# Optimization experiments

Hardware: AMD Instinct MI355X
Metric: run time of the kernel (lower is better)

Reference implementation:

```python
import jax, jax.numpy as jnp
import numpy as np

N = 4096      # number of nodes (len(batch_node))
K = 8         # number of adjacency channels
C = 256       # in_channels == out_channels
E = 131072    # number of edges (avg degree 32)


def setup_inputs() -> dict:
    key = jax.random.key(0)
    k1, k2, k3 = jax.random.split(key, 3)
    h = jax.random.normal(k1, (C, N), dtype=jnp.float32)
    X = jax.random.normal(k2, (E, K), dtype=jnp.float32)
    # sample unique (src, dst) pairs so the scatter-set has no duplicate writes
    rng = np.random.default_rng(0)
    flat = rng.choice(N * N, size=E, replace=False)
    edge_index = jnp.asarray(np.stack([flat // N, flat % N]).astype(np.int32))
    batch_node = jnp.zeros((N,), dtype=jnp.float32)
    # glorot uniform: stdv = sqrt(6 / (in + out))
    stdv = np.sqrt(6.0 / (C + C)).astype(np.float32)
    weight = jax.random.uniform(k3, (K, C, C), dtype=jnp.float32,
                                minval=-stdv, maxval=stdv)
    bias = jnp.zeros((C,), dtype=jnp.float32)
    return {"h": h, "X": X, "edge_index": edge_index,
            "batch_node": batch_node, "weight": weight, "bias": bias}


def reference(h, X, edge_index, batch_node, weight, bias):
    Kk = weight.shape[0]
    Nn = batch_node.shape[0]
    # scatter edge features into K dense [N, N] adjacency tensors
    resx = jnp.zeros((Kk, Nn, Nn), dtype=h.dtype)
    resx = resx.at[:, edge_index[0], edge_index[1]].set(X.T)
    # res[k] = h @ resx[k] : [K, C, N]
    res = jnp.einsum('cn,knm->kcm', h, resx)
    # sum_k weight[k] @ res[k] : [C, N]  (in_channels == out_channels)
    out = jnp.einsum('kio,kon->in', weight, res)
    # (res.T + bias).T == res + bias[:, None]
    return out + bias[:, None]
```

## Files before the change

### kernel.cpp

```cpp
#include <hip/hip_runtime.h>

constexpr int NN = 4096;
constexpr int KC = 8;
constexpr int CC = 256;
constexpr int NE = 131072;
constexpr int KK = KC * CC;
constexpr int CAP = 96;

typedef short bf16x8 __attribute__((ext_vector_type(8)));
typedef float f32x4 __attribute__((ext_vector_type(4)));

__device__ inline unsigned short f2bf(float f) {
    union { float f; unsigned int u; } v; v.f = f;
    unsigned int u = v.u;
    u += 0x7fffu + ((u >> 16) & 1u);
    return (unsigned short)(u >> 16);
}
__device__ inline float bf2f(unsigned short u) {
    union { unsigned int i; float f; } w; w.i = ((unsigned int)u) << 16; return w.f;
}

__global__ __launch_bounds__(256) void k_prep(
    const float* __restrict__ h, const float* __restrict__ w,
    unsigned short* __restrict__ ht, unsigned short* __restrict__ A,
    int* __restrict__ cursor) {
    int b = blockIdx.x;
    int t = threadIdx.x;
    if (b < 1024) {
        __shared__ float tile[32][33];
        int nb = b >> 3, cb = b & 7;
        int n0 = nb * 32, c0 = cb * 32;
        int tx = t & 31, ty = t >> 5;
#pragma unroll
        for (int j = 0; j < 32; j += 8)
            tile[ty + j][tx] = h[(size_t)(c0 + ty + j) * NN + n0 + tx];
        __syncthreads();
#pragma unroll
        for (int j = 0; j < 32; j += 8)
            ht[(size_t)(n0 + ty + j) * CC + c0 + tx] = f2bf(tile[tx][ty + j]);
    } else {
        int idx = (b - 1024) * 256 + t;
        if (idx < NN) cursor[idx] = 0;
        int o = idx & 255;
        int k = (idx >> 8) & 7;
        int i = idx >> 11;
        A[idx] = f2bf(w[(k << 16) | (i << 8) | o]);
    }
}

__global__ void k_fill(const int* __restrict__ edge_src, const int* __restrict__ edge_dst,
                       int* __restrict__ cursor, int2* __restrict__ bins) {
    int e = blockIdx.x * 256 + threadIdx.x;
    int d = edge_dst[e];
    int slot = atomicAdd(&cursor[d], 1);
    if (slot < CAP) bins[d * CAP + slot] = make_int2(e, edge_src[e]);
}

__device__ inline void agg_accum(f32x4 acc[KC], float4 v, float4 xa, float4 xb) {
    f32x4 vv = {v.x, v.y, v.z, v.w};
    acc[0] += xa.x * vv; acc[1] += xa.y * vv;
    acc[2] += xa.z * vv; acc[3] += xa.w * vv;
    acc[4] += xb.x * vv; acc[5] += xb.y * vv;
    acc[6] += xb.z * vv; acc[7] += xb.w * vv;
}

__global__ __launch_bounds__(256) void k_agg(
    const int* __restrict__ cursor, const int2* __restrict__ bins,
    const float* __restrict__ X, const unsigned short* __restrict__ ht,
    unsigned short* __restrict__ agg) {
    const int wid  = __builtin_amdgcn_readfirstlane(threadIdx.x >> 6);
    const int lane = threadIdx.x & 63;
    const int n = blockIdx.x * 4 + wid;
    int cnt = cursor[n];
    cnt = cnt > CAP ? CAP : cnt;
    const int p0 = n * CAP;
    const int p1 = p0 + cnt;
    const float4* X4 = reinterpret_cast<const float4*>(X);

    f32x4 acc[KC] = {};

    int p = p0;
    for (; p + 8 <= p1; p += 8) {
        int2 q[8];
        ushort4 u[8];
#pragma unroll
        for (int j = 0; j < 8; ++j) q[j] = bins[p + j];
#pragma unroll
        for (int j = 0; j < 8; ++j)
            u[j] = *(const ushort4*)(ht + (size_t)q[j].y * CC + 4 * lane);
#pragma unroll
        for (int j = 0; j < 8; ++j) {
            float4 v = {bf2f(u[j].x), bf2f(u[j].y), bf2f(u[j].z), bf2f(u[j].w)};
            agg_accum(acc, v, X4[q[j].x * 2], X4[q[j].x * 2 + 1]);
        }
    }
    for (; p < p1; ++p) {
        int2 q = bins[p];
        ushort4 u = *(const ushort4*)(ht + (size_t)q.y * CC + 4 * lane);
        float4 v = {bf2f(u.x), bf2f(u.y), bf2f(u.z), bf2f(u.w)};
        agg_accum(acc, v, X4[q.x * 2], X4[q.x * 2 + 1]);
    }

    unsigned short* op = agg + (size_t)n * KK + 4 * lane;
#pragma unroll
    for (int k = 0; k < KC; ++k) {
        ushort4 w;
        w.x = f2bf(acc[k][0]); w.y = f2bf(acc[k][1]);
        w.z = f2bf(acc[k][2]); w.w = f2bf(acc[k][3]);
        *reinterpret_cast<ushort4*>(op + k * CC) = w;
    }
}

__global__ __launch_bounds__(256) void k_gemm_mfma(
    const unsigned short* __restrict__ A, const unsigned short* __restrict__ B,
    const float* __restrict__ bias, float* __restrict__ out) {
    constexpr int BM = 64, BN = 32, BK = 64;
    constexpr int NT = KK / BK;
    __shared__ unsigned short As[2][BM][BK];
    __shared__ unsigned short Bs[2][BN][BK];
    const int tid  = threadIdx.x;
    const int wid  = tid >> 6;
    const int lane = tid & 63;

    const int raw = blockIdx.x;
    const int swz = (raw & 7) * 64 + (raw >> 3);
    const int i0 = (swz & 3) * BM;
    const int n0 = (swz >> 2) * BN;

    const int wm = (wid & 1) * 32;
    const int wn = (wid >> 1) * 16;

    const int lrow = lane >> 3;
    const int csrc = ((lane & 7) ^ lrow) * 8;

    f32x4 acc[2] = {};

#define STAGE(T, BUF)                                                              \
    do {                                                                           \
        int kc0_ = (T) * BK;                                                       \
        _Pragma("unroll")                                                          \
        for (int q = 0; q < 2; ++q) {                                              \
            int seg = wid + q * 4;                                                 \
            int row = seg * 8 + lrow;                                              \
            __builtin_amdgcn_global_load_lds(                                      \
                (const __attribute__((address_space(1))) void*)(                   \
                    A + (size_t)(i0 + row) * KK + kc0_ + csrc),                    \
                (__attribute__((address_space(3))) void*)(                         \
                    (char*)&As[BUF][0][0] + seg * 1024), 16, 0, 0);                \
        }                                                                          \
        {                                                                          \
            int row = wid * 8 + lrow;                                              \
            __builtin_amdgcn_global_load_lds(                                      \
                (const __attribute__((address_space(1))) void*)(                   \
                    B + (size_t)(n0 + row) * KK + kc0_ + csrc),                    \
                (__attribute__((address_space(3))) void*)(                         \
                    (char*)&Bs[BUF][0][0] + wid * 1024), 16, 0, 0);                \
        }                                                                          \
    } while (0)

    STAGE(0, 0);

    const int rA = wm + (lane & 15);
    const int rB = wn + (lane & 15);
    const int sw = lane & 7;
    const int chb = lane >> 4;

    for (int t = 0; t < NT; ++t) {
        int b = t & 1;
        if (t + 1 < NT) {
            STAGE(t + 1, b ^ 1);
            asm volatile("s_waitcnt vmcnt(3)" ::: "memory");
        } else {
            asm volatile("s_waitcnt vmcnt(0)" ::: "memory");
        }
        __builtin_amdgcn_s_barrier();
        asm volatile("" ::: "memory");

        const char* Ab = (const char*)&As[b][0][0];
        const char* Bb = (const char*)&Bs[b][0][0];
#pragma unroll
        for (int ks = 0; ks < BK; ks += 32) {
            const int ch = (ks >> 3) + chb;
            bf16x8 a0 = *(const bf16x8*)(Ab + rA * 128 + ((ch ^ sw) << 4));
            bf16x8 a1 = *(const bf16x8*)(Ab + (rA + 16) * 128 + ((ch ^ sw) << 4));
            bf16x8 b0 = *(const bf16x8*)(Bb + rB * 128 + ((ch ^ sw) << 4));
            acc[0] = __builtin_amdgcn_mfma_f32_16x16x32_bf16(a0, b0, acc[0], 0, 0, 0);
            acc[1] = __builtin_amdgcn_mfma_f32_16x16x32_bf16(a1, b0, acc[1], 0, 0, 0);
        }
        asm volatile("" ::: "memory");
        __builtin_amdgcn_s_barrier();
    }
#undef STAGE

    const int lr = (lane >> 4) * 4;
    const int lc = lane & 15;
#pragma unroll
    for (int mi = 0; mi < 2; ++mi) {
#pragma unroll
        for (int r = 0; r < 4; ++r) {
            int i = i0 + wm + mi * 16 + lr + r;
            out[(size_t)i * NN + n0 + wn + lc] = acc[mi][r] + bias[i];
        }
    }
}

extern "C" void kernel_launch(void* const* d_in, const int* in_sizes, int n_in,
                              void* d_out, int out_size, void* d_ws, size_t ws_size,
                              hipStream_t stream) {
    const float* h      = (const float*)d_in[0];
    const float* X      = (const float*)d_in[1];
    const int* edge_idx = (const int*)d_in[2];
    const float* weight = (const float*)d_in[4];
    const float* bias   = (const float*)d_in[5];
    float* out = (float*)d_out;

    const int* edge_src = edge_idx;
    const int* edge_dst = edge_idx + NE;

    char* ws = (char*)d_ws;
    unsigned short* ht   = (unsigned short*)(ws);
    unsigned short* Abf  = (unsigned short*)(ws + (2 << 20));
    unsigned short* agg  = (unsigned short*)(ws + (4 << 20));
    size_t meta = (size_t)(20 << 20);
    int* cursor = (int*)(ws + meta);
    int2* bins  = (int2*)(ws + meta + 65536);

    k_prep<<<3072, 256, 0, stream>>>(h, weight, ht, Abf, cursor);
    k_fill<<<NE / 256, 256, 0, stream>>>(edge_src, edge_dst, cursor, bins);
    k_agg<<<NN / 4, 256, 0, stream>>>(cursor, bins, X, ht, agg);
    k_gemm_mfma<<<512, 256, 0, stream>>>(Abf, agg, bias, out);
}
```

Measured before the change: 54.28 us.

## Vectorize weight conversion, scalarize edge indices, and enlarge GEMM N-tile with 512 threads

The weight bf16 conversion in k_prep now handles four elements per thread with float4 loads, which halves the block count. In k_agg the cursor count and edge/source indices are made wave-uniform via readfirstlane so addressing can use scalar registers. The GEMM moves to a 64x64 tile with 512 threads and 256 blocks, and each wave issues one A and one B async load per stage. The larger tile improves reuse of the A tile, at the cost of fewer blocks to spread across the CUs.

```diff
diff --git a/kernel.cpp b/kernel.cpp
--- a/kernel.cpp
+++ b/kernel.cpp
@@ -39,12 +39,14 @@
         for (int j = 0; j < 32; j += 8)
             ht[(size_t)(n0 + ty + j) * CC + c0 + tx] = f2bf(tile[tx][ty + j]);
     } else {
-        int idx = (b - 1024) * 256 + t;
-        if (idx < NN) cursor[idx] = 0;
-        int o = idx & 255;
-        int k = (idx >> 8) & 7;
-        int i = idx >> 11;
-        A[idx] = f2bf(w[(k << 16) | (i << 8) | o]);
+        int g = (b - 1024) * 256 + t;
+        if (g < NN) cursor[g] = 0;
+        int idx = g * 4;
+        int o = idx & 255, k = (idx >> 8) & 7, i = idx >> 11;
+        float4 wv = *reinterpret_cast<const float4*>(w + ((k << 16) | (i << 8) | o));
+        ushort4 av;
+        av.x = f2bf(wv.x); av.y = f2bf(wv.y); av.z = f2bf(wv.z); av.w = f2bf(wv.w);
+        *reinterpret_cast<ushort4*>(A + idx) = av;
     }
 }
 
@@ -71,7 +73,7 @@
     const int wid  = __builtin_amdgcn_readfirstlane(threadIdx.x >> 6);
     const int lane = threadIdx.x & 63;
     const int n = blockIdx.x * 4 + wid;
-    int cnt = cursor[n];
+    int cnt = __builtin_amdgcn_readfirstlane(cursor[n]);
     cnt = cnt > CAP ? CAP : cnt;
     const int p0 = n * CAP;
     const int p1 = p0 + cnt;
@@ -81,24 +83,30 @@
 
     int p = p0;
     for (; p + 8 <= p1; p += 8) {
-        int2 q[8];
+        int es[8], ss[8];
+#pragma unroll
+        for (int j = 0; j < 8; ++j) {
+            int2 qv = bins[p + j];
+            es[j] = __builtin_amdgcn_readfirstlane(qv.x);
+            ss[j] = __builtin_amdgcn_readfirstlane(qv.y);
+        }
         ushort4 u[8];
 #pragma unroll
-        for (int j = 0; j < 8; ++j) q[j] = bins[p + j];
-#pragma unroll
         for (int j = 0; j < 8; ++j)
-            u[j] = *(const ushort4*)(ht + (size_t)q[j].y * CC + 4 * lane);
+            u[j] = *(const ushort4*)(ht + (size_t)ss[j] * CC + 4 * lane);
 #pragma unroll
         for (int j = 0; j < 8; ++j) {
             float4 v = {bf2f(u[j].x), bf2f(u[j].y), bf2f(u[j].z), bf2f(u[j].w)};
-            agg_accum(acc, v, X4[q[j].x * 2], X4[q[j].x * 2 + 1]);
+            agg_accum(acc, v, X4[es[j] * 2], X4[es[j] * 2 + 1]);
         }
     }
     for (; p < p1; ++p) {
-        int2 q = bins[p];
-        ushort4 u = *(const ushort4*)(ht + (size_t)q.y * CC + 4 * lane);
+        int2 qv = bins[p];
+        int es = __builtin_amdgcn_readfirstlane(qv.x);
+        int ss = __builtin_amdgcn_readfirstlane(qv.y);
+        ushort4 u = *(const ushort4*)(ht + (size_t)ss * CC + 4 * lane);
         float4 v = {bf2f(u.x), bf2f(u.y), bf2f(u.z), bf2f(u.w)};
-        agg_accum(acc, v, X4[q.x * 2], X4[q.x * 2 + 1]);
+        agg_accum(acc, v, X4[es * 2], X4[es * 2 + 1]);
     }
 
     unsigned short* op = agg + (size_t)n * KK + 4 * lane;
@@ -111,10 +119,10 @@
     }
 }
 
-__global__ __launch_bounds__(256) void k_gemm_mfma(
+__global__ __launch_bounds__(512) void k_gemm_mfma(
     const unsigned short* __restrict__ A, const unsigned short* __restrict__ B,
     const float* __restrict__ bias, float* __restrict__ out) {
-    constexpr int BM = 64, BN = 32, BK = 64;
+    constexpr int BM = 64, BN = 64, BK = 64;
     constexpr int NT = KK / BK;
     __shared__ unsigned short As[2][BM][BK];
     __shared__ unsigned short Bs[2][BN][BK];
@@ -123,7 +131,7 @@
     const int lane = tid & 63;
 
     const int raw = blockIdx.x;
-    const int swz = (raw & 7) * 64 + (raw >> 3);
+    const int swz = (raw & 7) * 32 + (raw >> 3);
     const int i0 = (swz & 3) * BM;
     const int n0 = (swz >> 2) * BN;
 
@@ -138,24 +146,17 @@
 #define STAGE(T, BUF)                                                              \
     do {                                                                           \
         int kc0_ = (T) * BK;                                                       \
-        _Pragma("unroll")                                                          \
-        for (int q = 0; q < 2; ++q) {                                              \
-            int seg = wid + q * 4;                                                 \
-            int row = seg * 8 + lrow;                                              \
-            __builtin_amdgcn_global_load_lds(                                      \
-                (const __attribute__((address_space(1))) void*)(                   \
-                    A + (size_t)(i0 + row) * KK + kc0_ + csrc),                    \
-                (__attribute__((address_space(3))) void*)(                         \
-                    (char*)&As[BUF][0][0] + seg * 1024), 16, 0, 0);                \
-        }                                                                          \
-        {                                                                          \
-            int row = wid * 8 + lrow;                                              \
-            __builtin_amdgcn_global_load_lds(                                      \
-                (const __attribute__((address_space(1))) void*)(                   \
-                    B + (size_t)(n0 + row) * KK + kc0_ + csrc),                    \
-                (__attribute__((address_space(3))) void*)(                         \
-                    (char*)&Bs[BUF][0][0] + wid * 1024), 16, 0, 0);                \
-        }                                                                          \
+        int row = wid * 8 + lrow;                                                  \
+        __builtin_amdgcn_global_load_lds(                                          \
+            (const __attribute__((address_space(1))) void*)(                       \
+                A + (size_t)(i0 + row) * KK + kc0_ + csrc),                        \
+            (__attribute__((address_space(3))) void*)(                             \
+                (char*)&As[BUF][0][0] + wid * 1024), 16, 0, 0);                    \
+        __builtin_amdgcn_global_load_lds(                                          \
+            (const __attribute__((address_space(1))) void*)(                       \
+                B + (size_t)(n0 + row) * KK + kc0_ + csrc),                        \
+            (__attribute__((address_space(3))) void*)(                             \
+                (char*)&Bs[BUF][0][0] + wid * 1024), 16, 0, 0);                    \
     } while (0)
 
     STAGE(0, 0);
@@ -169,7 +170,7 @@
         int b = t & 1;
         if (t + 1 < NT) {
             STAGE(t + 1, b ^ 1);
-            asm volatile("s_waitcnt vmcnt(3)" ::: "memory");
+            asm volatile("s_waitcnt vmcnt(2)" ::: "memory");
         } else {
             asm volatile("s_waitcnt vmcnt(0)" ::: "memory");
         }
@@ -225,8 +226,8 @@
     int* cursor = (int*)(ws + meta);
     int2* bins  = (int2*)(ws + meta + 65536);
 
-    k_prep<<<3072, 256, 0, stream>>>(h, weight, ht, Abf, cursor);
+    k_prep<<<1536, 256, 0, stream>>>(h, weight, ht, Abf, cursor);
     k_fill<<<NE / 256, 256, 0, stream>>>(edge_src, edge_dst, cursor, bins);
     k_agg<<<NN / 4, 256, 0, stream>>>(cursor, bins, X, ht, agg);
-    k_gemm_mfma<<<512, 256, 0, stream>>>(Abf, agg, bias, out);
-}
+    k_gemm_mfma<<<256, 512, 0, stream>>>(Abf, agg, bias, out);
+}
```

Measured after the change: 56.40 us. 1.04x slower.

## Deepen GEMM LDS pipeline to four stages and vectorize prep and bin loads

Applied to the files above, without the earlier changes.

The GEMM moves from double buffering to a four-slot LDS ring with three tiles prefetched ahead, and the vmcnt waits are adjusted to match, so more global loads stay in flight. The weight-conversion part of the prep kernel now handles four elements per thread with float4 loads and ushort4 stores, which halves its block count. The aggregation kernel reads edge bins as int4 pairs instead of separate int2 loads. The extra LDS use per GEMM block may lower occupancy. The cursor zeroing now covers only the first NN threads of 512 blocks, so it still covers all NN entries.

```diff
diff --git a/kernel.cpp b/kernel.cpp
--- a/kernel.cpp
+++ b/kernel.cpp
@@ -39,12 +39,14 @@
         for (int j = 0; j < 32; j += 8)
             ht[(size_t)(n0 + ty + j) * CC + c0 + tx] = f2bf(tile[tx][ty + j]);
     } else {
-        int idx = (b - 1024) * 256 + t;
-        if (idx < NN) cursor[idx] = 0;
-        int o = idx & 255;
-        int k = (idx >> 8) & 7;
-        int i = idx >> 11;
-        A[idx] = f2bf(w[(k << 16) | (i << 8) | o]);
+        int g = (b - 1024) * 256 + t;
+        if (g < NN) cursor[g] = 0;
+        int idx = g * 4;
+        int o = idx & 255, k = (idx >> 8) & 7, i = idx >> 11;
+        float4 wv = *reinterpret_cast<const float4*>(w + ((k << 16) | (i << 8) | o));
+        ushort4 av;
+        av.x = f2bf(wv.x); av.y = f2bf(wv.y); av.z = f2bf(wv.z); av.w = f2bf(wv.w);
+        *reinterpret_cast<ushort4*>(A + idx) = av;
     }
 }
 
@@ -81,17 +83,18 @@
 
     int p = p0;
     for (; p + 8 <= p1; p += 8) {
-        int2 q[8];
+        const int4* b4 = reinterpret_cast<const int4*>(bins + p);
+        int4 r0 = b4[0], r1 = b4[1], r2 = b4[2], r3 = b4[3];
+        int es[8] = {r0.x, r0.z, r1.x, r1.z, r2.x, r2.z, r3.x, r3.z};
+        int ss[8] = {r0.y, r0.w, r1.y, r1.w, r2.y, r2.w, r3.y, r3.w};
         ushort4 u[8];
 #pragma unroll
-        for (int j = 0; j < 8; ++j) q[j] = bins[p + j];
-#pragma unroll
         for (int j = 0; j < 8; ++j)
-            u[j] = *(const ushort4*)(ht + (size_t)q[j].y * CC + 4 * lane);
+            u[j] = *(const ushort4*)(ht + (size_t)ss[j] * CC + 4 * lane);
 #pragma unroll
         for (int j = 0; j < 8; ++j) {
             float4 v = {bf2f(u[j].x), bf2f(u[j].y), bf2f(u[j].z), bf2f(u[j].w)};
-            agg_accum(acc, v, X4[q[j].x * 2], X4[q[j].x * 2 + 1]);
+            agg_accum(acc, v, X4[es[j] * 2], X4[es[j] * 2 + 1]);
         }
     }
     for (; p < p1; ++p) {
@@ -116,8 +119,8 @@
     const float* __restrict__ bias, float* __restrict__ out) {
     constexpr int BM = 64, BN = 32, BK = 64;
     constexpr int NT = KK / BK;
-    __shared__ unsigned short As[2][BM][BK];
-    __shared__ unsigned short Bs[2][BN][BK];
+    __shared__ unsigned short As[4][BM][BK];
+    __shared__ unsigned short Bs[4][BN][BK];
     const int tid  = threadIdx.x;
     const int wid  = tid >> 6;
     const int lane = tid & 63;
@@ -145,7 +148,7 @@
             __builtin_amdgcn_global_load_lds(                                      \
                 (const __attribute__((address_space(1))) void*)(                   \
                     A + (size_t)(i0 + row) * KK + kc0_ + csrc),                    \
-                (__attribute__((address_space(3))) void*)(                         \
+            (__attribute__((address_space(3))) void*)(                             \
                     (char*)&As[BUF][0][0] + seg * 1024), 16, 0, 0);                \
         }                                                                          \
         {                                                                          \
@@ -159,25 +162,26 @@
     } while (0)
 
     STAGE(0, 0);
+    STAGE(1, 1);
+    STAGE(2, 2);
 
     const int rA = wm + (lane & 15);
     const int rB = wn + (lane & 15);
     const int sw = lane & 7;
     const int chb = lane >> 4;
 
+#pragma unroll
     for (int t = 0; t < NT; ++t) {
-        int b = t & 1;
-        if (t + 1 < NT) {
-            STAGE(t + 1, b ^ 1);
-            asm volatile("s_waitcnt vmcnt(3)" ::: "memory");
-        } else {
-            asm volatile("s_waitcnt vmcnt(0)" ::: "memory");
-        }
+        if (t + 3 < NT) STAGE(t + 3, (t + 3) & 3);
+        if (t + 3 < NT)      asm volatile("s_waitcnt vmcnt(9)" ::: "memory");
+        else if (t + 2 < NT) asm volatile("s_waitcnt vmcnt(6)" ::: "memory");
+        else if (t + 1 < NT) asm volatile("s_waitcnt vmcnt(3)" ::: "memory");
+        else                 asm volatile("s_waitcnt vmcnt(0)" ::: "memory");
         __builtin_amdgcn_s_barrier();
         asm volatile("" ::: "memory");
 
-        const char* Ab = (const char*)&As[b][0][0];
-        const char* Bb = (const char*)&Bs[b][0][0];
+        const char* Ab = (const char*)&As[t & 3][0][0];
+        const char* Bb = (const char*)&Bs[t & 3][0][0];
 #pragma unroll
         for (int ks = 0; ks < BK; ks += 32) {
             const int ch = (ks >> 3) + chb;
@@ -225,7 +229,7 @@
     int* cursor = (int*)(ws + meta);
     int2* bins  = (int2*)(ws + meta + 65536);
 
-    k_prep<<<3072, 256, 0, stream>>>(h, weight, ht, Abf, cursor);
+    k_prep<<<1536, 256, 0, stream>>>(h, weight, ht, Abf, cursor);
     k_fill<<<NE / 256, 256, 0, stream>>>(edge_src, edge_dst, cursor, bins);
     k_agg<<<NN / 4, 256, 0, stream>>>(cursor, bins, X, ht, agg);
     k_gemm_mfma<<<512, 256, 0, stream>>>(Abf, agg, bias, out);
```

Measured after the change: 56.08 us. 3.3% more time.
